# Kernel tuning notes

Hardware: AMD Instinct MI355X
Metric: run time of the kernel (lower is better)

## Reference

```python
import jax, jax.numpy as jnp
import numpy as np


def _pdist2squared(x, y):
    # x: [B, 3, N], y: [B, 3, M] -> squared pairwise dists [B, N, M]
    xx = jnp.sum(x * x, axis=1)[:, :, None]          # [B, N, 1]
    yy = jnp.sum(y * y, axis=1)[:, None, :]          # [B, 1, M]
    dist = xx + yy - 2.0 * jnp.einsum('bdn,bdm->bnm', x, y)
    dist = jnp.where(jnp.isnan(dist), 0.0, dist)     # dist[dist != dist] = 0
    return jnp.maximum(dist, 0.0)                    # clamp to [0, inf)


def setup_inputs() -> dict:
    key = jax.random.key(0)
    k1, k2, k3 = jax.random.split(key, 3)
    B, N, M, C = 4, 16384, 4096, 64
    return {
        'points': jax.random.normal(k1, (B, 3, N), dtype=jnp.float32),
        'new_points': jax.random.normal(k2, (B, 3, M), dtype=jnp.float32),
        'features': jax.random.normal(k3, (B, C, N), dtype=jnp.float32),
        'num_samples': 32,
    }


def reference(points, new_points, features, num_samples):
    # kNN indices: smallest num_samples dists along N for each query m
    dist = _pdist2squared(points, new_points)            # [B, N, M]
    neg = -jnp.transpose(dist, (0, 2, 1))                # [B, M, N]
    _, idx = jax.lax.top_k(neg, num_samples)             # [B, M, K]

    # group_gather_by_index: gather along last axis by idx -> [B, C, M, K]
    def gather(t):
        return jnp.take_along_axis(t[:, :, None, :], idx[:, None, :, :], axis=3)

    grouped_points = gather(points) - new_points[:, :, :, None]   # [B, 3, M, K]
    grouped_features = gather(features)                            # [B, C, M, K]
    return jnp.concatenate([grouped_points, grouped_features], axis=1)
```

## Files before the change

kernel.cpp:

```cpp
#include <hip/hip_runtime.h>

static constexpr int Bn = 4;
static constexpr int Nn = 16384;
static constexpr int Mn = 4096;
static constexpr int Cn = 64;
static constexpr int Kn = 32;

static constexpr int CHUNK   = 2048;
static constexpr int WPB     = 8;
static constexpr int THREADS = WPB * 64;
static constexpr int NCHUNK  = Nn / CHUNK;
static constexpr int NGROUP  = CHUNK / 256;
static constexpr int LSLOTS  = 40;

typedef unsigned long long ull;
typedef unsigned int u32;

__device__ __forceinline__ u32 dpp_shr1(u32 v) {
  return (u32)__builtin_amdgcn_update_dpp((int)v, (int)v, 0x138, 0xf, 0xf, false);
}
__device__ __forceinline__ u32 rdlane(u32 v, int l) {
  return (u32)__builtin_amdgcn_readlane((int)v, l);
}
__device__ __forceinline__ float rdlane_f(float v, int l) {
  return __uint_as_float(rdlane(__float_as_uint(v), l));
}

__device__ __forceinline__ ull sort64_asc(ull key, int lane) {
#pragma unroll
  for (int k = 2; k <= 64; k <<= 1) {
#pragma unroll
    for (int j = k >> 1; j > 0; j >>= 1) {
      const ull other = __shfl_xor(key, j);
      const bool keep_min = ((lane & j) == 0) == ((lane & k) == 0);
      const bool take = keep_min ? (other < key) : (other > key);
      key = take ? other : key;
    }
  }
  return key;
}

__device__ __forceinline__ void insert40(float kj, u32 ki,
                                         float& lst_s, u32& lst_i,
                                         float& tau_s, int lane) {
  const int pos = (int)__popcll(__ballot(lst_s >= kj));
  const float shd = __uint_as_float(dpp_shr1(__float_as_uint(lst_s)));
  const u32  shi = dpp_shr1(lst_i);
  float nd = (lane == pos) ? kj : shd;
  u32   ni = (lane == pos) ? ki : shi;
  nd = (lane < pos) ? lst_s : nd;
  ni = (lane < pos) ? lst_i : ni;
  if (lane < LSLOTS) { lst_s = nd; lst_i = ni; }
  tau_s = rdlane_f(lst_s, LSLOTS - 1);
}

#define SUBW_INS(SX, JOFF)                                                   \
  {                                                                          \
    ull mm = __ballot((SX) > tau_s);                                         \
    while (mm) {                                                             \
      const int src = (int)__builtin_ctzll(mm);                              \
      const float k = rdlane_f((SX), src);                                   \
      if (k > tau_s)                                                         \
        insert40(k, nb + ((u32)src << 2) + (JOFF), lst_s, lst_i, tau_s, lane);\
      mm &= mm - 1;                                                          \
      mm &= __ballot((SX) > tau_s);                                          \
    }                                                                        \
  }

__global__ __launch_bounds__(256) void transpose_f(
    const float* __restrict__ F, float* __restrict__ FT) {
  __shared__ float t[64][65];
  const int tid = threadIdx.x;
  const int bid = blockIdx.x;
  const int xcd = bid & 7;
  const int b   = xcd >> 1;
  const int nt  = (bid >> 3) * 2 + (xcd & 1);
  const float* Fb = F + (size_t)b * Cn * Nn;
  float* FTb = FT + (size_t)b * Nn * Cn;
  for (int sub = 0; sub < 4; ++sub) {
    const int nbase = nt * 256 + sub * 64;
#pragma unroll
    for (int i = 0; i < 16; ++i) {
      const int c = (tid >> 6) + 4 * i;
      t[c][tid & 63] = Fb[(size_t)c * Nn + nbase + (tid & 63)];
    }
    __syncthreads();
#pragma unroll
    for (int i = 0; i < 16; ++i) {
      const int nn = (tid >> 6) + 4 * i;
      FTb[(size_t)(nbase + nn) * Cn + (tid & 63)] = t[tid & 63][nn];
    }
    __syncthreads();
  }
}

__global__ __launch_bounds__(THREADS, 6) void knn_group(
    const float* __restrict__ P,
    const float* __restrict__ Q,
    const float* __restrict__ FT,
    float* __restrict__ out)
{
#pragma clang fp contract(off)
  __shared__ float lds[4][CHUNK];

  const int tid  = threadIdx.x;
  const int lane = tid & 63;
  const int wid  = tid >> 6;
  const int bid  = blockIdx.x;
  const int xcd  = bid & 7;
  const int b    = xcd >> 1;
  const int tile = (bid >> 3) * 2 + (xcd & 1);
  const int m    = tile * WPB + wid;

  const float* Pb = P + (size_t)b * 3 * Nn;
  const float* Qb = Q + (size_t)b * 3 * Mn;

  const float qx = Qb[m];
  const float qy = Qb[Mn + m];
  const float qz = Qb[2 * Mn + m];
  const float yyq = (qx * qx + qy * qy) + qz * qz;

  const int t4 = tid * 4;

  float lst_s = -__builtin_inff();
  u32   lst_i = 0u;
  float tau_s = -__builtin_inff();

  {
    float4 vx = *(const float4*)(Pb + t4);
    float4 vy = *(const float4*)(Pb + Nn + t4);
    float4 vz = *(const float4*)(Pb + 2 * Nn + t4);
    float4 vh;
    vh.x = -0.5f * ((vx.x * vx.x + vy.x * vy.x) + vz.x * vz.x);
    vh.y = -0.5f * ((vx.y * vx.y + vy.y * vy.y) + vz.y * vz.y);
    vh.z = -0.5f * ((vx.z * vx.z + vy.z * vy.z) + vz.z * vz.z);
    vh.w = -0.5f * ((vx.w * vx.w + vy.w * vy.w) + vz.w * vz.w);
    *(float4*)&lds[0][t4] = vx;
    *(float4*)&lds[1][t4] = vy;
    *(float4*)&lds[2][t4] = vz;
    *(float4*)&lds[3][t4] = vh;
  }
  __syncthreads();

  {
    const float x = lds[0][lane];
    const float y = lds[1][lane];
    const float z = lds[2][lane];
    const float h = lds[3][lane];
    const float s = fmaf(z, qz, fmaf(y, qy, fmaf(x, qx, h)));
    const u32 sb = __float_as_uint(s);
    const u32 os = sb ^ (((int)sb < 0) ? 0xFFFFFFFFu : 0x80000000u);
    ull key = (((ull)(~os)) << 32) | (u32)lane;
    key = sort64_asc(key, lane);
    const int i0 = (int)(key & 0xFFFFFFFFull);
    const float sv = __shfl(s, i0);
    if (lane < LSLOTS) { lst_s = sv; lst_i = (u32)i0; }
    tau_s = rdlane_f(lst_s, LSLOTS - 1);
  }

  for (int ch = 0; ch < NCHUNK; ++ch) {
    const int n0 = ch * CHUNK;

    float4 nx, ny, nz;
    if (ch + 1 < NCHUNK) {
      nx = *(const float4*)(Pb + (n0 + CHUNK) + t4);
      ny = *(const float4*)(Pb + Nn + (n0 + CHUNK) + t4);
      nz = *(const float4*)(Pb + 2 * Nn + (n0 + CHUNK) + t4);
    }

#pragma unroll
    for (int g = 0; g < NGROUP; ++g) {
      const int p = g * 256 + lane * 4;
      const float4 rx = *(const float4*)&lds[0][p];
      const float4 ry = *(const float4*)&lds[1][p];
      const float4 rz = *(const float4*)&lds[2][p];
      const float4 rh = *(const float4*)&lds[3][p];

      float s0 = fmaf(rz.x, qz, fmaf(ry.x, qy, fmaf(rx.x, qx, rh.x)));
      float s1 = fmaf(rz.y, qz, fmaf(ry.y, qy, fmaf(rx.y, qx, rh.y)));
      float s2 = fmaf(rz.z, qz, fmaf(ry.z, qy, fmaf(rx.z, qx, rh.z)));
      float s3 = fmaf(rz.w, qz, fmaf(ry.w, qy, fmaf(rx.w, qx, rh.w)));

      if (ch == 0 && g == 0 && lane < 16) {
        s0 = s1 = s2 = s3 = -__builtin_inff();
      }

      const float smax = fmaxf(fmaxf(s0, s1), fmaxf(s2, s3));
      if (__any(smax > tau_s)) {
        const u32 nb = (u32)(n0 + g * 256);
        SUBW_INS(s0, 0u)
        SUBW_INS(s1, 1u)
        SUBW_INS(s2, 2u)
        SUBW_INS(s3, 3u)
      }
    }
    __syncthreads();

    if (ch + 1 < NCHUNK) {
      float4 vh;
      vh.x = -0.5f * ((nx.x * nx.x + ny.x * ny.x) + nz.x * nz.x);
      vh.y = -0.5f * ((nx.y * nx.y + ny.y * ny.y) + nz.y * nz.y);
      vh.z = -0.5f * ((nx.z * nx.z + ny.z * ny.z) + nz.z * nz.z);
      vh.w = -0.5f * ((nx.w * nx.w + ny.w * ny.w) + nz.w * nz.w);
      *(float4*)&lds[0][t4] = nx;
      *(float4*)&lds[1][t4] = ny;
      *(float4*)&lds[2][t4] = nz;
      *(float4*)&lds[3][t4] = vh;
      __syncthreads();
    }
  }

  ull key;
  {
    const int idx = (int)lst_i;
    const float x = Pb[idx];
    const float y = Pb[Nn + idx];
    const float z = Pb[2 * Nn + idx];
    const float xx = (x * x + y * y) + z * z;
    const float dot = fmaf(z, qz, fmaf(y, qy, x * qx));
    const float d = fmaxf((xx + yyq) - 2.0f * dot, 0.0f);
    key = (lane < LSLOTS)
            ? ((((ull)__float_as_uint(d)) << 32) | (u32)idx)
            : ~0ull;
    key = sort64_asc(key, lane);
  }

  const size_t MK = (size_t)Mn * Kn;
  float* outb = out + (size_t)b * (3 + Cn) * MK;

  if (lane < 32) {
    const int idx = (int)(key & 0xFFFFFFFFull);
    const float px = Pb[idx];
    const float py = Pb[Nn + idx];
    const float pz = Pb[2 * Nn + idx];
    outb[0 * MK + (size_t)m * Kn + lane] = px - qx;
    outb[1 * MK + (size_t)m * Kn + lane] = py - qy;
    outb[2 * MK + (size_t)m * Kn + lane] = pz - qz;
  }

  const float* FTb = FT + (size_t)b * Nn * Cn;
  const int r  = lane & 15;
  const int qh = lane >> 4;
#pragma unroll
  for (int p2 = 0; p2 < 2; ++p2) {
    const int k = p2 * 16 + r;
    const int idxk = (int)(__shfl(key, k) & 0xFFFFFFFFull);
    const float* row = FTb + (size_t)idxk * Cn;
    float4 v[4];
#pragma unroll
    for (int i = 0; i < 4; ++i)
      v[i] = *(const float4*)(row + (qh + 4 * i) * 4);
#pragma unroll
    for (int i = 0; i < 4; ++i) {
      const int c = (qh + 4 * i) * 4;
      float* o = outb + (size_t)(3 + c) * MK + (size_t)m * Kn + k;
      o[0 * MK] = v[i].x;
      o[1 * MK] = v[i].y;
      o[2 * MK] = v[i].z;
      o[3 * MK] = v[i].w;
    }
  }
}

extern "C" void kernel_launch(void* const* d_in, const int* in_sizes, int n_in,
                              void* d_out, int out_size, void* d_ws, size_t ws_size,
                              hipStream_t stream) {
  (void)in_sizes; (void)n_in; (void)out_size; (void)ws_size;
  const float* P = (const float*)d_in[0];
  const float* Q = (const float*)d_in[1];
  const float* F = (const float*)d_in[2];
  float* out = (float*)d_out;
  float* FT  = (float*)d_ws;

  hipLaunchKernelGGL(transpose_f, dim3(256), dim3(256), 0, stream, F, FT);
  hipLaunchKernelGGL(knn_group, dim3(Bn * Mn / WPB), dim3(THREADS), 0, stream,
                     P, Q, FT, out);
}
```

Baseline: 188.5 us.

## Replace brute-force kNN scan with uniform-grid spatial binning and shell search

Builds a 16^3 uniform grid per batch (bbox, histogram, scan, scatter kernels) and has each query wave visit cells in expanding Chebyshev shells, stopping once the shell distance bound exceeds the 32nd-best distance. This replaces scanning all 16384 points per query with a local search over nearby bins, using a full-scan fallback when the shells run out. It adds several small preprocessing launches, atomics and irregular gathers, and needs enough workspace; otherwise the old brute-force kernel runs.

Measured after the change: 236.6 us. +25.5%, slower.

```diff
diff --git a/kernel.cpp b/kernel.cpp
--- a/kernel.cpp
+++ b/kernel.cpp
@@ -6,16 +6,20 @@
 static constexpr int Cn = 64;
 static constexpr int Kn = 32;
 
-static constexpr int CHUNK   = 2048;
 static constexpr int WPB     = 8;
 static constexpr int THREADS = WPB * 64;
-static constexpr int NCHUNK  = Nn / CHUNK;
-static constexpr int NGROUP  = CHUNK / 256;
 static constexpr int LSLOTS  = 40;
+static constexpr int G       = 16;
+static constexpr int DMAX    = 6;
+static constexpr int NTAB    = 2197;
+static constexpr int BUF     = 1024;
+static constexpr float EPS   = 4e-3f;
 
 typedef unsigned long long ull;
 typedef unsigned int u32;
 
+#define NEG_INF (-__builtin_inff())
+
 __device__ __forceinline__ u32 dpp_shr1(u32 v) {
   return (u32)__builtin_amdgcn_update_dpp((int)v, (int)v, 0x138, 0xf, 0xf, false);
 }
@@ -24,6 +28,14 @@
 }
 __device__ __forceinline__ float rdlane_f(float v, int l) {
   return __uint_as_float(rdlane(__float_as_uint(v), l));
+}
+
+__device__ __forceinline__ u32 fenc(float f) {
+  u32 u = __float_as_uint(f);
+  return (u >> 31) ? ~u : (u | 0x80000000u);
+}
+__device__ __forceinline__ float fdec(u32 u) {
+  return __uint_as_float((u >> 31) ? (u ^ 0x80000000u) : ~u);
 }
 
 __device__ __forceinline__ ull sort64_asc(ull key, int lane) {
@@ -40,10 +52,15 @@
   return key;
 }
 
-__device__ __forceinline__ void insert40(float kj, u32 ki,
-                                         float& lst_s, u32& lst_i,
-                                         float& tau_s, int lane) {
-  const int pos = (int)__popcll(__ballot(lst_s >= kj));
+__device__ __forceinline__ bool better(float s, u32 i, float ts, u32 ti) {
+  return (s > ts) || (s == ts && i < ti);
+}
+
+__device__ __forceinline__ void ins40(float kj, u32 ki,
+                                      float& lst_s, u32& lst_i,
+                                      float& tau_s, u32& tau_i, int lane) {
+  const bool above = (lst_s > kj) || (lst_s == kj && lst_i < ki);
+  const int pos = (int)__popcll(__ballot(above));
   const float shd = __uint_as_float(dpp_shr1(__float_as_uint(lst_s)));
   const u32  shi = dpp_shr1(lst_i);
   float nd = (lane == pos) ? kj : shd;
@@ -52,20 +69,38 @@
   ni = (lane < pos) ? lst_i : ni;
   if (lane < LSLOTS) { lst_s = nd; lst_i = ni; }
   tau_s = rdlane_f(lst_s, LSLOTS - 1);
-}
-
-#define SUBW_INS(SX, JOFF)                                                   \
-  {                                                                          \
-    ull mm = __ballot((SX) > tau_s);                                         \
-    while (mm) {                                                             \
-      const int src = (int)__builtin_ctzll(mm);                              \
-      const float k = rdlane_f((SX), src);                                   \
-      if (k > tau_s)                                                         \
-        insert40(k, nb + ((u32)src << 2) + (JOFF), lst_s, lst_i, tau_s, lane);\
-      mm &= mm - 1;                                                          \
-      mm &= __ballot((SX) > tau_s);                                          \
-    }                                                                        \
-  }
+  tau_i = rdlane(lst_i, LSLOTS - 1);
+}
+
+struct ShellTab {
+  int start[DMAX + 2];
+  u32 off[NTAB];
+};
+constexpr ShellTab mk_tab() {
+  ShellTab t{};
+  int p = 0;
+  for (int d = 0; d <= DMAX; ++d) {
+    t.start[d] = p;
+    for (int dz = -d; dz <= d; ++dz)
+      for (int dy = -d; dy <= d; ++dy)
+        for (int dx = -d; dx <= d; ++dx) {
+          int ax = dx < 0 ? -dx : dx;
+          int ay = dy < 0 ? -dy : dy;
+          int az = dz < 0 ? -dz : dz;
+          int ch = ax > ay ? ax : ay; ch = ch > az ? ch : az;
+          if (ch == d)
+            t.off[p++] = (u32)((dx + 8) | ((dy + 8) << 8) | ((dz + 8) << 16));
+        }
+  }
+  t.start[DMAX + 1] = p;
+  return t;
+}
+__constant__ ShellTab g_tab = mk_tab();
+
+__device__ __forceinline__ int cellc(float v, float lo, float iv) {
+  int c = (int)((v - lo) * iv);
+  return c < 0 ? 0 : (c > G - 1 ? G - 1 : c);
+}
 
 __global__ __launch_bounds__(256) void transpose_f(
     const float* __restrict__ F, float* __restrict__ FT) {
@@ -94,14 +129,112 @@
   }
 }
 
-__global__ __launch_bounds__(THREADS, 6) void knn_group(
-    const float* __restrict__ P,
-    const float* __restrict__ Q,
-    const float* __restrict__ FT,
-    float* __restrict__ out)
-{
+__global__ __launch_bounds__(1024) void k_init(u32* cursor, u32* bbox) {
+  const int tid = threadIdx.x;
+  for (int i = tid; i < Bn * 4097; i += 1024) cursor[i] = 0u;
+  if (tid < Bn * 8) bbox[tid] = ((tid & 7) < 3) ? 0xFFFFFFFFu : 0u;
+}
+
+__global__ __launch_bounds__(256) void k_bbox(const float* __restrict__ P,
+                                              u32* bbox) {
+  const int gid = blockIdx.x * 256 + threadIdx.x;
+  const int b = gid >> 14, i = gid & 16383;
+  const float* Pb = P + (size_t)b * 3 * Nn;
+  u32 ex = fenc(Pb[i]), ey = fenc(Pb[Nn + i]), ez = fenc(Pb[2 * Nn + i]);
+  u32 mnx = ex, mny = ey, mnz = ez, mxx = ex, mxy = ey, mxz = ez;
+#pragma unroll
+  for (int j = 1; j < 64; j <<= 1) {
+    u32 t;
+    t = (u32)__shfl_xor((int)mnx, j); mnx = mnx < t ? mnx : t;
+    t = (u32)__shfl_xor((int)mny, j); mny = mny < t ? mny : t;
+    t = (u32)__shfl_xor((int)mnz, j); mnz = mnz < t ? mnz : t;
+    t = (u32)__shfl_xor((int)mxx, j); mxx = mxx > t ? mxx : t;
+    t = (u32)__shfl_xor((int)mxy, j); mxy = mxy > t ? mxy : t;
+    t = (u32)__shfl_xor((int)mxz, j); mxz = mxz > t ? mxz : t;
+  }
+  if ((threadIdx.x & 63) == 0) {
+    atomicMin(&bbox[b * 8 + 0], mnx);
+    atomicMin(&bbox[b * 8 + 1], mny);
+    atomicMin(&bbox[b * 8 + 2], mnz);
+    atomicMax(&bbox[b * 8 + 3], mxx);
+    atomicMax(&bbox[b * 8 + 4], mxy);
+    atomicMax(&bbox[b * 8 + 5], mxz);
+  }
+}
+
+__device__ __forceinline__ int binof(float x, float y, float z,
+                                     const u32* bb) {
+  const float b0x = fdec(bb[0]), b0y = fdec(bb[1]), b0z = fdec(bb[2]);
+  const float b1x = fdec(bb[3]), b1y = fdec(bb[4]), b1z = fdec(bb[5]);
+  const float ivx = (float)G / (b1x - b0x);
+  const float ivy = (float)G / (b1y - b0y);
+  const float ivz = (float)G / (b1z - b0z);
+  const int cx = cellc(x, b0x, ivx);
+  const int cy = cellc(y, b0y, ivy);
+  const int cz = cellc(z, b0z, ivz);
+  return (cz * G + cy) * G + cx;
+}
+
+__global__ __launch_bounds__(256) void k_hist(const float* __restrict__ P,
+                                              const u32* __restrict__ bbox,
+                                              u32* cursor) {
+  const int gid = blockIdx.x * 256 + threadIdx.x;
+  const int b = gid >> 14, i = gid & 16383;
+  const float* Pb = P + (size_t)b * 3 * Nn;
+  const int bin = binof(Pb[i], Pb[Nn + i], Pb[2 * Nn + i], bbox + b * 8);
+  atomicAdd(&cursor[b * 4097 + bin], 1u);
+}
+
+__global__ __launch_bounds__(1024) void k_scan(u32* cursor, u32* binStart) {
+  __shared__ u32 sm[1024];
+  const int b = blockIdx.x, tid = threadIdx.x;
+  u32* cur = cursor + b * 4097;
+  u32* bs  = binStart + b * 4097;
+  u32 v[4], loc = 0;
+#pragma unroll
+  for (int j = 0; j < 4; ++j) { v[j] = cur[tid * 4 + j]; loc += v[j]; }
+  sm[tid] = loc;
+  __syncthreads();
+  for (int off = 1; off < 1024; off <<= 1) {
+    const u32 t = (tid >= off) ? sm[tid - off] : 0u;
+    __syncthreads();
+    sm[tid] += t;
+    __syncthreads();
+  }
+  u32 s = sm[tid] - loc;
+#pragma unroll
+  for (int j = 0; j < 4; ++j) {
+    bs[tid * 4 + j] = s;
+    cur[tid * 4 + j] = s;
+    s += v[j];
+  }
+  if (tid == 1023) bs[4096] = s;
+}
+
+__global__ __launch_bounds__(256) void k_scatter(const float* __restrict__ P,
+                                                 const u32* __restrict__ bbox,
+                                                 u32* cursor,
+                                                 float4* __restrict__ pts4,
+                                                 u32* __restrict__ pidx) {
 #pragma clang fp contract(off)
-  __shared__ float lds[4][CHUNK];
+  const int gid = blockIdx.x * 256 + threadIdx.x;
+  const int b = gid >> 14, i = gid & 16383;
+  const float* Pb = P + (size_t)b * 3 * Nn;
+  const float x = Pb[i], y = Pb[Nn + i], z = Pb[2 * Nn + i];
+  const int bin = binof(x, y, z, bbox + b * 8);
+  const u32 pos = atomicAdd(&cursor[b * 4097 + bin], 1u);
+  const float h = -0.5f * ((x * x + y * y) + z * z);
+  pts4[((size_t)b << 14) + pos] = make_float4(x, y, z, h);
+  pidx[((size_t)b << 14) + pos] = (u32)i;
+}
+
+__global__ __launch_bounds__(THREADS, 4) void knn_bin(
+    const float* __restrict__ P, const float* __restrict__ Q,
+    const float* __restrict__ FT, const float4* __restrict__ pts4,
+    const u32* __restrict__ pidx, const u32* __restrict__ binStart,
+    const u32* __restrict__ bbox, float* __restrict__ out) {
+#pragma clang fp contract(off)
+  __shared__ u32 sbuf[WPB][BUF];
 
   const int tid  = threadIdx.x;
   const int lane = tid & 63;
@@ -120,11 +253,233 @@
   const float qz = Qb[2 * Mn + m];
   const float yyq = (qx * qx + qy * qy) + qz * qz;
 
+  const u32* bb = bbox + b * 8;
+  const float b0x = fdec(bb[0]), b0y = fdec(bb[1]), b0z = fdec(bb[2]);
+  const float b1x = fdec(bb[3]), b1y = fdec(bb[4]), b1z = fdec(bb[5]);
+  const float ivx = (float)G / (b1x - b0x);
+  const float ivy = (float)G / (b1y - b0y);
+  const float ivz = (float)G / (b1z - b0z);
+  const float hmin = fminf((b1x - b0x), fminf((b1y - b0y), (b1z - b0z))) *
+                     (1.0f / G);
+  const int cix = cellc(qx, b0x, ivx);
+  const int ciy = cellc(qy, b0y, ivy);
+  const int ciz = cellc(qz, b0z, ivz);
+
+  const u32* bs = binStart + b * 4097;
+  const float4* pp4 = pts4 + ((size_t)b << 14);
+  const u32* pid4 = pidx + ((size_t)b << 14);
+  u32* wbuf = sbuf[wid];
+
+  float lst_s = NEG_INF; u32 lst_i = 0u;
+  float tau_s = NEG_INF; u32 tau_i = 0xFFFFFFFFu;
+  bool first = true, done = false;
+
+  for (int d = 0; d <= DMAX + 1; ++d) {
+    if (d >= 2) {
+      const float s32 = rdlane_f(lst_s, 31);
+      if (s32 > NEG_INF) {
+        const float gd = (float)(d - 1) * hmin;
+        if (gd * gd > yyq - 2.0f * s32 + EPS) { done = true; break; }
+      }
+    }
+    if (d > DMAX) break;
+    const int cs = g_tab.start[d], ce = g_tab.start[d + 1];
+    for (int cb = cs; cb < ce; cb += 64) {
+      const int cn = ce - cb;
+      u32 st = 0, cnt = 0;
+      if (lane < cn) {
+        const u32 e = g_tab.off[cb + lane];
+        const int cx = cix + (int)(e & 0xFFu) - 8;
+        const int cy = ciy + (int)((e >> 8) & 0xFFu) - 8;
+        const int cz = ciz + (int)((e >> 16) & 0xFFu) - 8;
+        if ((u32)cx < (u32)G && (u32)cy < (u32)G && (u32)cz < (u32)G) {
+          const int bin = (cz * G + cy) * G + cx;
+          st = bs[bin];
+          cnt = bs[bin + 1] - st;
+        }
+      }
+      u32 incl = cnt;
+#pragma unroll
+      for (int j = 1; j < 64; j <<= 1) {
+        const u32 t = (u32)__shfl_up((int)incl, j);
+        if (lane >= j) incl += t;
+      }
+      const u32 total = rdlane(incl, 63);
+      const u32 excl = incl - cnt;
+      for (u32 slice = 0; slice < total; slice += BUF) {
+        const u32 se = total < slice + BUF ? total : slice + BUF;
+        const u32 wlo = excl > slice ? excl : slice;
+        const u32 whi = (excl + cnt) < se ? (excl + cnt) : se;
+        for (u32 t = wlo; t < whi; ++t) wbuf[t - slice] = st + (t - excl);
+        asm volatile("s_waitcnt lgkmcnt(0)" ::: "memory");
+        const u32 ns = se - slice;
+        for (u32 t0 = 0; t0 < ns; t0 += 64) {
+          const bool act = (t0 + (u32)lane) < ns;
+          u32 rdix = t0 + (u32)lane;
+          if (!act) rdix = 0;
+          const u32 ppos = wbuf[rdix];
+          const float4 pv = pp4[ppos];
+          const u32 pid = pid4[ppos];
+          float s = fmaf(pv.z, qz, fmaf(pv.y, qy, fmaf(pv.x, qx, pv.w)));
+          if (first) {
+            first = false;
+            const float ss = act ? s : NEG_INF;
+            const u32 os = fenc(ss);
+            ull key = (((ull)(~os)) << 32) | (ull)pid;
+            key = sort64_asc(key, lane);
+            const u32 osr = ~((u32)(key >> 32));
+            const float sr = fdec(osr);
+            if (lane < LSLOTS) { lst_s = sr; lst_i = (u32)(key & 0xFFFFFFFFull); }
+            tau_s = rdlane_f(lst_s, LSLOTS - 1);
+            tau_i = rdlane(lst_i, LSLOTS - 1);
+          } else {
+            if (!act) s = __builtin_nanf("");
+            ull mm = __ballot(better(s, pid, tau_s, tau_i));
+            while (mm) {
+              const int src = (int)__builtin_ctzll(mm);
+              mm &= mm - 1;
+              const float kj = rdlane_f(s, src);
+              const u32 ki = rdlane(pid, src);
+              if (better(kj, ki, tau_s, tau_i))
+                ins40(kj, ki, lst_s, lst_i, tau_s, tau_i, lane);
+              mm &= __ballot(better(s, pid, tau_s, tau_i));
+            }
+          }
+        }
+      }
+    }
+  }
+
+  if (!done) {
+    lst_s = NEG_INF; lst_i = 0u; tau_s = NEG_INF; tau_i = 0xFFFFFFFFu;
+    for (u32 t0 = 0; t0 < (u32)Nn; t0 += 64) {
+      const u32 ppos = t0 + (u32)lane;
+      const float4 pv = pp4[ppos];
+      const u32 pid = pid4[ppos];
+      const float s = fmaf(pv.z, qz, fmaf(pv.y, qy, fmaf(pv.x, qx, pv.w)));
+      ull mm = __ballot(better(s, pid, tau_s, tau_i));
+      while (mm) {
+        const int src = (int)__builtin_ctzll(mm);
+        mm &= mm - 1;
+        const float kj = rdlane_f(s, src);
+        const u32 ki = rdlane(pid, src);
+        if (better(kj, ki, tau_s, tau_i))
+          ins40(kj, ki, lst_s, lst_i, tau_s, tau_i, lane);
+        mm &= __ballot(better(s, pid, tau_s, tau_i));
+      }
+    }
+  }
+
+  ull key;
+  {
+    const int idx = (int)lst_i;
+    const float x = Pb[idx];
+    const float y = Pb[Nn + idx];
+    const float z = Pb[2 * Nn + idx];
+    const float xx = (x * x + y * y) + z * z;
+    const float dot = fmaf(z, qz, fmaf(y, qy, x * qx));
+    const float dd = fmaxf((xx + yyq) - 2.0f * dot, 0.0f);
+    key = (lane < LSLOTS && lst_s > NEG_INF)
+            ? ((((ull)__float_as_uint(dd)) << 32) | (u32)idx)
+            : ~0ull;
+    key = sort64_asc(key, lane);
+  }
+
+  const size_t MK = (size_t)Mn * Kn;
+  float* outb = out + (size_t)b * (3 + Cn) * MK;
+
+  if (lane < 32) {
+    const int idx = (int)(key & 0xFFFFFFFFull);
+    const float px = Pb[idx];
+    const float py = Pb[Nn + idx];
+    const float pz = Pb[2 * Nn + idx];
+    outb[0 * MK + (size_t)m * Kn + lane] = px - qx;
+    outb[1 * MK + (size_t)m * Kn + lane] = py - qy;
+    outb[2 * MK + (size_t)m * Kn + lane] = pz - qz;
+  }
+
+  const float* FTb = FT + (size_t)b * Nn * Cn;
+  const int r  = lane & 15;
+  const int qh = lane >> 4;
+#pragma unroll
+  for (int p2 = 0; p2 < 2; ++p2) {
+    const int k = p2 * 16 + r;
+    const int idxk = (int)(__shfl(key, k) & 0xFFFFFFFFull);
+    const float* row = FTb + (size_t)idxk * Cn;
+    float4 v[4];
+#pragma unroll
+    for (int i = 0; i < 4; ++i)
+      v[i] = *(const float4*)(row + (qh + 4 * i) * 4);
+#pragma unroll
+    for (int i = 0; i < 4; ++i) {
+      const int c = (qh + 4 * i) * 4;
+      float* o = outb + (size_t)(3 + c) * MK + (size_t)m * Kn + k;
+      o[0 * MK] = v[i].x;
+      o[1 * MK] = v[i].y;
+      o[2 * MK] = v[i].z;
+      o[3 * MK] = v[i].w;
+    }
+  }
+}
+
+static constexpr int CHUNK  = 2048;
+static constexpr int NCHUNK = Nn / CHUNK;
+static constexpr int NGROUP = CHUNK / 256;
+
+__device__ __forceinline__ void ins40s(float kj, u32 ki,
+                                       float& lst_s, u32& lst_i,
+                                       float& tau_s, int lane) {
+  const int pos = (int)__popcll(__ballot(lst_s >= kj));
+  const float shd = __uint_as_float(dpp_shr1(__float_as_uint(lst_s)));
+  const u32  shi = dpp_shr1(lst_i);
+  float nd = (lane == pos) ? kj : shd;
+  u32   ni = (lane == pos) ? ki : shi;
+  nd = (lane < pos) ? lst_s : nd;
+  ni = (lane < pos) ? lst_i : ni;
+  if (lane < LSLOTS) { lst_s = nd; lst_i = ni; }
+  tau_s = rdlane_f(lst_s, LSLOTS - 1);
+}
+
+#define SUBW_INS(SX, JOFF)                                                   \
+  {                                                                          \
+    ull mm = __ballot((SX) > tau_s);                                         \
+    while (mm) {                                                             \
+      const int src = (int)__builtin_ctzll(mm);                              \
+      const float k = rdlane_f((SX), src);                                   \
+      if (k > tau_s)                                                         \
+        ins40s(k, nb + ((u32)src << 2) + (JOFF), lst_s, lst_i, tau_s, lane); \
+      mm &= mm - 1;                                                          \
+      mm &= __ballot((SX) > tau_s);                                          \
+    }                                                                        \
+  }
+
+__global__ __launch_bounds__(THREADS, 6) void knn_full(
+    const float* __restrict__ P, const float* __restrict__ Q,
+    const float* __restrict__ FT, float* __restrict__ out) {
+#pragma clang fp contract(off)
+  __shared__ float lds[4][CHUNK];
+
+  const int tid  = threadIdx.x;
+  const int lane = tid & 63;
+  const int wid  = tid >> 6;
+  const int bid  = blockIdx.x;
+  const int xcd  = bid & 7;
+  const int b    = xcd >> 1;
+  const int tile = (bid >> 3) * 2 + (xcd & 1);
+  const int m    = tile * WPB + wid;
+
+  const float* Pb = P + (size_t)b * 3 * Nn;
+  const float* Qb = Q + (size_t)b * 3 * Mn;
+
+  const float qx = Qb[m];
+  const float qy = Qb[Mn + m];
+  const float qz = Qb[2 * Mn + m];
+  const float yyq = (qx * qx + qy * qy) + qz * qz;
+
   const int t4 = tid * 4;
-
-  float lst_s = -__builtin_inff();
+  float lst_s = NEG_INF;
   u32   lst_i = 0u;
-  float tau_s = -__builtin_inff();
+  float tau_s = NEG_INF;
 
   {
     float4 vx = *(const float4*)(Pb + t4);
@@ -148,11 +503,10 @@
     const float z = lds[2][lane];
     const float h = lds[3][lane];
     const float s = fmaf(z, qz, fmaf(y, qy, fmaf(x, qx, h)));
-    const u32 sb = __float_as_uint(s);
-    const u32 os = sb ^ (((int)sb < 0) ? 0xFFFFFFFFu : 0x80000000u);
+    const u32 os = fenc(s);
     ull key = (((ull)(~os)) << 32) | (u32)lane;
     key = sort64_asc(key, lane);
-    const int i0 = (int)(key & 0xFFFFFFFFull);
+    const int i0 = (int)(key & 0xffffffffull);
     const float sv = __shfl(s, i0);
     if (lane < LSLOTS) { lst_s = sv; lst_i = (u32)i0; }
     tau_s = rdlane_f(lst_s, LSLOTS - 1);
@@ -160,14 +514,12 @@
 
   for (int ch = 0; ch < NCHUNK; ++ch) {
     const int n0 = ch * CHUNK;
-
     float4 nx, ny, nz;
     if (ch + 1 < NCHUNK) {
       nx = *(const float4*)(Pb + (n0 + CHUNK) + t4);
       ny = *(const float4*)(Pb + Nn + (n0 + CHUNK) + t4);
       nz = *(const float4*)(Pb + 2 * Nn + (n0 + CHUNK) + t4);
     }
-
 #pragma unroll
     for (int g = 0; g < NGROUP; ++g) {
       const int p = g * 256 + lane * 4;
@@ -175,16 +527,13 @@
       const float4 ry = *(const float4*)&lds[1][p];
       const float4 rz = *(const float4*)&lds[2][p];
       const float4 rh = *(const float4*)&lds[3][p];
-
       float s0 = fmaf(rz.x, qz, fmaf(ry.x, qy, fmaf(rx.x, qx, rh.x)));
       float s1 = fmaf(rz.y, qz, fmaf(ry.y, qy, fmaf(rx.y, qx, rh.y)));
       float s2 = fmaf(rz.z, qz, fmaf(ry.z, qy, fmaf(rx.z, qx, rh.z)));
       float s3 = fmaf(rz.w, qz, fmaf(ry.w, qy, fmaf(rx.w, qx, rh.w)));
-
       if (ch == 0 && g == 0 && lane < 16) {
-        s0 = s1 = s2 = s3 = -__builtin_inff();
+        s0 = s1 = s2 = s3 = NEG_INF;
       }
-
       const float smax = fmaxf(fmaxf(s0, s1), fmaxf(s2, s3));
       if (__any(smax > tau_s)) {
         const u32 nb = (u32)(n0 + g * 256);
@@ -195,7 +544,6 @@
       }
     }
     __syncthreads();
-
     if (ch + 1 < NCHUNK) {
       float4 vh;
       vh.x = -0.5f * ((nx.x * nx.x + ny.x * ny.x) + nz.x * nz.x);
@@ -219,7 +567,7 @@
     const float xx = (x * x + y * y) + z * z;
     const float dot = fmaf(z, qz, fmaf(y, qy, x * qx));
     const float d = fmaxf((xx + yyq) - 2.0f * dot, 0.0f);
-    key = (lane < LSLOTS)
+    key = (lane < LSLOTS && lst_s > NEG_INF)
             ? ((((ull)__float_as_uint(d)) << 32) | (u32)idx)
             : ~0ull;
     key = sort64_asc(key, lane);
@@ -227,7 +575,6 @@
 
   const size_t MK = (size_t)Mn * Kn;
   float* outb = out + (size_t)b * (3 + Cn) * MK;
-
   if (lane < 32) {
     const int idx = (int)(key & 0xFFFFFFFFull);
     const float px = Pb[idx];
@@ -237,7 +584,6 @@
     outb[1 * MK + (size_t)m * Kn + lane] = py - qy;
     outb[2 * MK + (size_t)m * Kn + lane] = pz - qz;
   }
-
   const float* FTb = FT + (size_t)b * Nn * Cn;
   const int r  = lane & 15;
   const int qh = lane >> 4;
@@ -265,14 +611,40 @@
 extern "C" void kernel_launch(void* const* d_in, const int* in_sizes, int n_in,
                               void* d_out, int out_size, void* d_ws, size_t ws_size,
                               hipStream_t stream) {
-  (void)in_sizes; (void)n_in; (void)out_size; (void)ws_size;
+  (void)in_sizes; (void)n_in; (void)out_size;
   const float* P = (const float*)d_in[0];
   const float* Q = (const float*)d_in[1];
   const float* F = (const float*)d_in[2];
   float* out = (float*)d_out;
-  float* FT  = (float*)d_ws;
-
+  char* ws = (char*)d_ws;
+
+  const size_t FT_OFF  = 0;
+  const size_t PTS_OFF = 16777216;
+  const size_t IDX_OFF = PTS_OFF + 1048576;
+  const size_t BS_OFF  = IDX_OFF + 262144;
+  const size_t CUR_OFF = BS_OFF + (size_t)Bn * 4097 * 4;
+  const size_t BB_OFF  = CUR_OFF + (size_t)Bn * 4097 * 4;
+  const size_t NEED    = BB_OFF + (size_t)Bn * 8 * 4;
+
+  float* FT = (float*)(ws + FT_OFF);
   hipLaunchKernelGGL(transpose_f, dim3(256), dim3(256), 0, stream, F, FT);
-  hipLaunchKernelGGL(knn_group, dim3(Bn * Mn / WPB), dim3(THREADS), 0, stream,
-                     P, Q, FT, out);
-}
+
+  if (ws_size >= NEED) {
+    float4* pts4 = (float4*)(ws + PTS_OFF);
+    u32* pidx = (u32*)(ws + IDX_OFF);
+    u32* bs   = (u32*)(ws + BS_OFF);
+    u32* cur  = (u32*)(ws + CUR_OFF);
+    u32* bb   = (u32*)(ws + BB_OFF);
+    hipLaunchKernelGGL(k_init,    dim3(1),   dim3(1024), 0, stream, cur, bb);
+    hipLaunchKernelGGL(k_bbox,    dim3(256), dim3(256),  0, stream, P, bb);
+    hipLaunchKernelGGL(k_hist,    dim3(256), dim3(256),  0, stream, P, bb, cur);
+    hipLaunchKernelGGL(k_scan,    dim3(Bn),  dim3(1024), 0, stream, cur, bs);
+    hipLaunchKernelGGL(k_scatter, dim3(256), dim3(256),  0, stream, P, bb, cur,
+                       pts4, pidx);
+    hipLaunchKernelGGL(knn_bin, dim3(Bn * Mn / WPB), dim3(THREADS), 0, stream,
+                       P, Q, FT, pts4, pidx, bs, bb, out);
+  } else {
+    hipLaunchKernelGGL(knn_full, dim3(Bn * Mn / WPB), dim3(THREADS), 0, stream,
+                       P, Q, FT, out);
+  }
+}
```
